# Performance work log

Measured on AMD Instinct MI355X. Metric: run time of the kernel, lower is better.

The kernel has to match this reference:

```python
import jax, jax.numpy as jnp
import numpy as np

B, N, C, O, R = 8, 1024, 768, 768, 16  # batch, tokens, in_features, out_features, rank


def setup_inputs() -> dict:
    key = jax.random.key(0)
    k1, k2, k3, k4 = jax.random.split(key, 4)
    x = jax.random.normal(k1, (B, N, C), dtype=jnp.float32)
    coef = jax.random.normal(k2, (N, R), dtype=jnp.float32)
    # params: weight (out_features, in_features, rank), bias (out_features, rank)
    weight = 0.02 * jax.random.normal(k3, (O, C, R), dtype=jnp.float32)
    bias = 0.02 * jax.random.normal(k4, (O, R), dtype=jnp.float32)
    return {"x": x, "coef": coef, "weight": weight, "bias": bias}


def reference(x, coef, weight, bias):
    # Original math: per-token weight W_n[o,c] = sum_r coef[n,r] * weight[o,c,r]
    #                out[b,n,o] = sum_c x[b,n,c] * W_n[o,c] + sum_r coef[n,r]*bias[o,r]
    # Fused form: contract in_features first, rank last; avoids the (N,O,C) tensor.
    t = jnp.einsum('bnc,ocr->bnor', x, weight)   # (B,N,O,R)
    out = jnp.einsum('bnor,nr->bno', t, coef)    # (B,N,O)
    out = out + coef @ bias.T                    # (N,O) broadcast over batch
    return out
```

## Files before the change

kernel.cpp:

```cpp
#include <hip/hip_runtime.h>

#define BB 8
#define NN 1024
#define CC 768
#define OO 768
#define RR 16
#define MM (BB*NN)
#define KK (CC*RR)
#define BM 128
#define BO 128
#define BK 64
#define KTILES (KK/BK)

typedef __bf16 bf16x8 __attribute__((ext_vector_type(8)));
typedef float  f32x4  __attribute__((ext_vector_type(4)));

__device__ static __forceinline__ void gl_lds16(const void* g, void* l) {
    __builtin_amdgcn_global_load_lds(
        (const __attribute__((address_space(1))) void*)g,
        (__attribute__((address_space(3))) void*)l,
        16, 0, 0);
}

__global__ __launch_bounds__(256) void k_prep(const float* __restrict__ w,
                                              const float* __restrict__ coef,
                                              const float* __restrict__ bias,
                                              __bf16* __restrict__ wbf,
                                              float* __restrict__ bterm) {
    long id = blockIdx.x;
    if (id < 4608) {
        long u = (id * 256 + threadIdx.x) * 8;
        float4 a = *(const float4*)(w + u);
        float4 b = *(const float4*)(w + u + 4);
        bf16x8 v = {(__bf16)a.x, (__bf16)a.y, (__bf16)a.z, (__bf16)a.w,
                    (__bf16)b.x, (__bf16)b.y, (__bf16)b.z, (__bf16)b.w};
        *(bf16x8*)(wbf + u) = v;
    } else {
        int i = (int)(id - 4608) * 256 + threadIdx.x;
        int n = i / OO, o = i - n * OO;
        float s = 0.f;
#pragma unroll
        for (int r = 0; r < RR; ++r) s += coef[n * RR + r] * bias[o * RR + r];
        bterm[i] = s;
    }
}

__global__ __launch_bounds__(256, 2) void k_gemm(const float* __restrict__ x,
                                                 const float* __restrict__ coef,
                                                 const __bf16* __restrict__ wbf,
                                                 const float* __restrict__ bterm,
                                                 float* __restrict__ out) {
    __shared__ __bf16 lA[BM * BK];
    __shared__ __bf16 lB[BO * BK];

    const int tid = threadIdx.x;

    int id    = blockIdx.x;
    int xcd   = id & 7;
    int slot  = id >> 3;
    int otile = slot >> 3;
    int mtile = xcd * 8 + (slot & 7);
    const int m0 = mtile * BM, o0 = otile * BO;

    const int am     = tid & 127;
    const int ahalf  = tid >> 7;
    const int m_glob = m0 + am;
    const int n_idx  = m_glob & (NN - 1);
    const float* xrow = x + (long)m_glob * CC;

    float cf[16];
#pragma unroll
    for (int r = 0; r < 16; r += 4) {
        float4 t4 = *(const float4*)(coef + n_idx * RR + r);
        cf[r] = t4.x; cf[r + 1] = t4.y; cf[r + 2] = t4.z; cf[r + 3] = t4.w;
    }

    const int lane = tid & 63, wave = tid >> 6;
    const int wm = (wave & 1) * 64, wo = (wave >> 1) * 64;
    const int lrow = lane & 15, quad = lane >> 4;

    f32x4 acc[4][4] = {};

    float2 x2 = *(const float2*)(xrow + 2 * ahalf);

#pragma unroll 1
    for (int kt = 0; kt < KTILES; ++kt) {
#pragma unroll
        for (int s = 0; s < 4; ++s) {
            int u = s * 256 + tid;
            int row = u >> 3, cl = u & 7;
            int g = cl ^ (row & 7);
            const __bf16* gp = wbf + (long)(o0 + row) * KK + kt * BK + g * 8;
            gl_lds16(gp, ((char*)lB) + u * 16);
        }
        float2 x2n = x2;
        if (kt + 1 < KTILES) x2n = *(const float2*)(xrow + (kt + 1) * 4 + 2 * ahalf);
#pragma unroll
        for (int ci = 0; ci < 2; ++ci) {
            float xv = (ci == 0) ? x2.x : x2.y;
            int c_local = 2 * ahalf + ci;
#pragma unroll
            for (int rh = 0; rh < 2; ++rh) {
                bf16x8 v;
#pragma unroll
                for (int j = 0; j < 8; ++j) v[j] = (__bf16)(xv * cf[rh * 8 + j]);
                int kb  = c_local * 2 + rh;
                int kbs = kb ^ (am & 7);
                *(bf16x8*)(&lA[am * BK + kbs * 8]) = v;
            }
        }
        x2 = x2n;
        __syncthreads();

#pragma unroll
        for (int ks = 0; ks < 2; ++ks) {
            bf16x8 af[4], bfr[4];
            int kb = ks * 4 + quad;
#pragma unroll
            for (int im = 0; im < 4; ++im) {
                int row = wm + im * 16 + lrow;
                af[im] = *(const bf16x8*)(&lA[row * BK + (kb ^ (row & 7)) * 8]);
            }
#pragma unroll
            for (int io = 0; io < 4; ++io) {
                int row = wo + io * 16 + lrow;
                bfr[io] = *(const bf16x8*)(&lB[row * BK + (kb ^ (row & 7)) * 8]);
            }
#pragma unroll
            for (int im = 0; im < 4; ++im)
#pragma unroll
                for (int io = 0; io < 4; ++io)
                    acc[im][io] = __builtin_amdgcn_mfma_f32_16x16x32_bf16(
                        af[im], bfr[io], acc[im][io], 0, 0, 0);
        }
        __syncthreads();
    }

    const int nbase = m0 & (NN - 1);
#pragma unroll
    for (int im = 0; im < 4; ++im) {
#pragma unroll
        for (int io = 0; io < 4; ++io) {
            int o = o0 + wo + io * 16 + lrow;
#pragma unroll
            for (int r = 0; r < 4; ++r) {
                int moff = wm + im * 16 + quad * 4 + r;
                long m = m0 + moff;
                out[m * OO + o] = acc[im][io][r] + bterm[(nbase + moff) * OO + o];
            }
        }
    }
}

__global__ void k_naive(const float* __restrict__ x, const float* __restrict__ coef,
                        const float* __restrict__ w, const float* __restrict__ bias,
                        float* __restrict__ out) {
    long i = (long)blockIdx.x * 256 + threadIdx.x;
    if (i >= (long)MM * OO) return;
    int o = (int)(i % OO);
    long m = i / OO;
    int n = (int)(m & (NN - 1));
    float cf[16];
#pragma unroll
    for (int r = 0; r < 16; ++r) cf[r] = coef[n * RR + r];
    const float* xr = x + m * CC;
    const float* wr = w + (long)o * CC * RR;
    float s = 0.f;
    for (int c = 0; c < CC; ++c) {
        float t = 0.f;
#pragma unroll
        for (int r = 0; r < 16; ++r) t += cf[r] * wr[c * RR + r];
        s += xr[c] * t;
    }
    float bs = 0.f;
#pragma unroll
    for (int r = 0; r < 16; ++r) bs += cf[r] * bias[o * RR + r];
    out[i] = s + bs;
}

extern "C" void kernel_launch(void* const* d_in, const int* in_sizes, int n_in,
                              void* d_out, int out_size, void* d_ws, size_t ws_size,
                              hipStream_t stream) {
    const float* x    = (const float*)d_in[0];
    const float* coef = (const float*)d_in[1];
    const float* w    = (const float*)d_in[2];
    const float* bias = (const float*)d_in[3];
    float* out = (float*)d_out;

    const size_t wbf_bytes = (size_t)OO * KK * sizeof(__bf16);
    const size_t bt_bytes  = (size_t)NN * OO * sizeof(float);

    if (ws_size >= wbf_bytes + bt_bytes) {
        __bf16* wbf  = (__bf16*)d_ws;
        float*  btrm = (float*)((char*)d_ws + wbf_bytes);
        k_prep<<<7680, 256, 0, stream>>>(w, coef, bias, wbf, btrm);
        k_gemm<<<384, 256, 0, stream>>>(x, coef, wbf, btrm, out);
    } else {
        k_naive<<<(int)(((long)MM * OO + 255) / 256), 256, 0, stream>>>(x, coef, w, bias, out);
    }
}
```

Measured before the change: 284.9 us.

## Build A fragments in registers, double-buffer B tile, halve output tile width

The x⊗coef A operand is no longer staged through LDS. Each lane now forms its bf16 MFMA A fragment directly in registers from a preloaded x float4 and its own coef slice, and only the weight tile goes through LDS, now double-buffered so the next tile's global-to-LDS load overlaps compute. The output tile shrinks to 64 columns, doubling the grid to 768 blocks and raising the occupancy hint to 3. The goal is to remove the A-tile LDS writes and reads and one barrier per k-step. The costs are redundant A-fragment conversion across waves, less B reuse per block and more global weight traffic.

```diff
diff --git a/kernel.cpp b/kernel.cpp
--- a/kernel.cpp
+++ b/kernel.cpp
@@ -1,14 +1,13 @@
 #include <hip/hip_runtime.h>
 
-#define BB 8
 #define NN 1024
 #define CC 768
 #define OO 768
 #define RR 16
-#define MM (BB*NN)
+#define MM 8192
 #define KK (CC*RR)
 #define BM 128
-#define BO 128
+#define BO 64
 #define BK 64
 #define KTILES (KK/BK)
 
@@ -38,20 +37,24 @@
     } else {
         int i = (int)(id - 4608) * 256 + threadIdx.x;
         int n = i / OO, o = i - n * OO;
+        const float4* cp = (const float4*)(coef + n * RR);
+        const float4* bp = (const float4*)(bias + o * RR);
         float s = 0.f;
 #pragma unroll
-        for (int r = 0; r < RR; ++r) s += coef[n * RR + r] * bias[o * RR + r];
+        for (int q = 0; q < 4; ++q) {
+            float4 c4 = cp[q], b4 = bp[q];
+            s += c4.x * b4.x + c4.y * b4.y + c4.z * b4.z + c4.w * b4.w;
+        }
         bterm[i] = s;
     }
 }
 
-__global__ __launch_bounds__(256, 2) void k_gemm(const float* __restrict__ x,
+__global__ __launch_bounds__(256, 3) void k_gemm(const float* __restrict__ x,
                                                  const float* __restrict__ coef,
                                                  const __bf16* __restrict__ wbf,
                                                  const float* __restrict__ bterm,
                                                  float* __restrict__ out) {
-    __shared__ __bf16 lA[BM * BK];
-    __shared__ __bf16 lB[BO * BK];
+    __shared__ __bf16 lB[2][BO * BK];
 
     const int tid = threadIdx.x;
 
@@ -62,91 +65,91 @@
     int mtile = xcd * 8 + (slot & 7);
     const int m0 = mtile * BM, o0 = otile * BO;
 
-    const int am     = tid & 127;
-    const int ahalf  = tid >> 7;
-    const int m_glob = m0 + am;
-    const int n_idx  = m_glob & (NN - 1);
-    const float* xrow = x + (long)m_glob * CC;
-
-    float cf[16];
-#pragma unroll
-    for (int r = 0; r < 16; r += 4) {
-        float4 t4 = *(const float4*)(coef + n_idx * RR + r);
-        cf[r] = t4.x; cf[r + 1] = t4.y; cf[r + 2] = t4.z; cf[r + 3] = t4.w;
-    }
-
     const int lane = tid & 63, wave = tid >> 6;
-    const int wm = (wave & 1) * 64, wo = (wave >> 1) * 64;
+    const int wm = (wave & 1) * 64, wo = (wave >> 1) * 32;
     const int lrow = lane & 15, quad = lane >> 4;
-
-    f32x4 acc[4][4] = {};
-
-    float2 x2 = *(const float2*)(xrow + 2 * ahalf);
-
-#pragma unroll 1
-    for (int kt = 0; kt < KTILES; ++kt) {
-#pragma unroll
-        for (int s = 0; s < 4; ++s) {
+    const int qh = quad >> 1, ql = quad & 1;
+
+    float cf8[4][8];
+    const float* xrow[4];
+#pragma unroll
+    for (int f = 0; f < 4; ++f) {
+        int m = m0 + wm + f * 16 + lrow;
+        int n = m & (NN - 1);
+#pragma unroll
+        for (int j = 0; j < 8; j += 4) {
+            float4 t = *(const float4*)(coef + n * RR + ql * 8 + j);
+            cf8[f][j] = t.x; cf8[f][j + 1] = t.y; cf8[f][j + 2] = t.z; cf8[f][j + 3] = t.w;
+        }
+        xrow[f] = x + (long)m * CC;
+    }
+
+    auto stage = [&](int kt, int buf) {
+#pragma unroll
+        for (int s = 0; s < 2; ++s) {
             int u = s * 256 + tid;
             int row = u >> 3, cl = u & 7;
             int g = cl ^ (row & 7);
             const __bf16* gp = wbf + (long)(o0 + row) * KK + kt * BK + g * 8;
-            gl_lds16(gp, ((char*)lB) + u * 16);
-        }
-        float2 x2n = x2;
-        if (kt + 1 < KTILES) x2n = *(const float2*)(xrow + (kt + 1) * 4 + 2 * ahalf);
-#pragma unroll
-        for (int ci = 0; ci < 2; ++ci) {
-            float xv = (ci == 0) ? x2.x : x2.y;
-            int c_local = 2 * ahalf + ci;
-#pragma unroll
-            for (int rh = 0; rh < 2; ++rh) {
-                bf16x8 v;
-#pragma unroll
-                for (int j = 0; j < 8; ++j) v[j] = (__bf16)(xv * cf[rh * 8 + j]);
-                int kb  = c_local * 2 + rh;
-                int kbs = kb ^ (am & 7);
-                *(bf16x8*)(&lA[am * BK + kbs * 8]) = v;
+            gl_lds16(gp, ((char*)&lB[buf][0]) + u * 16);
+        }
+    };
+
+    f32x4 acc[4][2] = {};
+
+    stage(0, 0);
+    float4 x4[4];
+#pragma unroll
+    for (int f = 0; f < 4; ++f) x4[f] = *(const float4*)(xrow[f]);
+    __syncthreads();
+
+#pragma unroll 1
+    for (int kt = 0; kt < KTILES; ++kt) {
+        const int cur = kt & 1;
+        if (kt + 1 < KTILES) stage(kt + 1, cur ^ 1);
+        float4 x4n[4];
+        const int ktn = (kt + 1 < KTILES) ? kt + 1 : kt;
+#pragma unroll
+        for (int f = 0; f < 4; ++f) x4n[f] = *(const float4*)(xrow[f] + ktn * 4);
+
+#pragma unroll
+        for (int ks = 0; ks < 2; ++ks) {
+            bf16x8 bfr[2];
+            const int kb = ks * 4 + quad;
+#pragma unroll
+            for (int io = 0; io < 2; ++io) {
+                int row = wo + io * 16 + lrow;
+                bfr[io] = *(const bf16x8*)(&lB[cur][row * BK + ((kb ^ (row & 7)) * 8)]);
             }
-        }
-        x2 = x2n;
+#pragma unroll
+            for (int f = 0; f < 4; ++f) {
+                float xs = ks ? (qh ? x4[f].w : x4[f].z)
+                              : (qh ? x4[f].y : x4[f].x);
+                bf16x8 af;
+#pragma unroll
+                for (int j = 0; j < 8; ++j) af[j] = (__bf16)(xs * cf8[f][j]);
+#pragma unroll
+                for (int io = 0; io < 2; ++io)
+                    acc[f][io] = __builtin_amdgcn_mfma_f32_16x16x32_bf16(
+                        af, bfr[io], acc[f][io], 0, 0, 0);
+            }
+        }
+#pragma unroll
+        for (int f = 0; f < 4; ++f) x4[f] = x4n[f];
         __syncthreads();
-
-#pragma unroll
-        for (int ks = 0; ks < 2; ++ks) {
-            bf16x8 af[4], bfr[4];
-            int kb = ks * 4 + quad;
-#pragma unroll
-            for (int im = 0; im < 4; ++im) {
-                int row = wm + im * 16 + lrow;
-                af[im] = *(const bf16x8*)(&lA[row * BK + (kb ^ (row & 7)) * 8]);
-            }
-#pragma unroll
-            for (int io = 0; io < 4; ++io) {
-                int row = wo + io * 16 + lrow;
-                bfr[io] = *(const bf16x8*)(&lB[row * BK + (kb ^ (row & 7)) * 8]);
-            }
-#pragma unroll
-            for (int im = 0; im < 4; ++im)
-#pragma unroll
-                for (int io = 0; io < 4; ++io)
-                    acc[im][io] = __builtin_amdgcn_mfma_f32_16x16x32_bf16(
-                        af[im], bfr[io], acc[im][io], 0, 0, 0);
-        }
-        __syncthreads();
-    }
-
-    const int nbase = m0 & (NN - 1);
-#pragma unroll
-    for (int im = 0; im < 4; ++im) {
-#pragma unroll
-        for (int io = 0; io < 4; ++io) {
+    }
+
+#pragma unroll
+    for (int f = 0; f < 4; ++f) {
+#pragma unroll
+        for (int io = 0; io < 2; ++io) {
             int o = o0 + wo + io * 16 + lrow;
 #pragma unroll
             for (int r = 0; r < 4; ++r) {
-                int moff = wm + im * 16 + quad * 4 + r;
+                int moff = wm + f * 16 + quad * 4 + r;
                 long m = m0 + moff;
-                out[m * OO + o] = acc[im][io][r] + bterm[(nbase + moff) * OO + o];
+                int n = (int)(m & (NN - 1));
+                out[m * OO + o] = acc[f][io][r] + bterm[(long)n * OO + o];
             }
         }
     }
@@ -194,7 +197,7 @@
         __bf16* wbf  = (__bf16*)d_ws;
         float*  btrm = (float*)((char*)d_ws + wbf_bytes);
         k_prep<<<7680, 256, 0, stream>>>(w, coef, bias, wbf, btrm);
-        k_gemm<<<384, 256, 0, stream>>>(x, coef, wbf, btrm, out);
+        k_gemm<<<768, 256, 0, stream>>>(x, coef, wbf, btrm, out);
     } else {
         k_naive<<<(int)(((long)MM * OO + 255) / 256), 256, 0, stream>>>(x, coef, w, bias, out);
     }
```

Result: slower. 405.5 us (+42.4%).

## Split GEMM K dimension in two with atomic accumulation into zeroed output

Applied to the files above, without the earlier changes.

Splits the long K reduction (C*R) into two halves, doubling the grid from 384 to 768 blocks so all CUs get more work and better occupancy (launch bounds raised to 3 blocks/CU). The output is zeroed in the prep kernel and each half accumulates via float atomicAdd, with only the first half adding the bias term. The bias-term computation is also vectorized with float4 loads. This trades the extra output zeroing pass and atomic write traffic for improved parallelism and load balance.

```diff
diff --git a/kernel.cpp b/kernel.cpp
--- a/kernel.cpp
+++ b/kernel.cpp
@@ -1,16 +1,17 @@
 #include <hip/hip_runtime.h>
 
-#define BB 8
 #define NN 1024
 #define CC 768
 #define OO 768
 #define RR 16
-#define MM (BB*NN)
+#define MM 8192
 #define KK (CC*RR)
 #define BM 128
 #define BO 128
 #define BK 64
 #define KTILES (KK/BK)
+#define KSPLIT 2
+#define KHALF (KTILES/KSPLIT)
 
 typedef __bf16 bf16x8 __attribute__((ext_vector_type(8)));
 typedef float  f32x4  __attribute__((ext_vector_type(4)));
@@ -26,7 +27,8 @@
                                               const float* __restrict__ coef,
                                               const float* __restrict__ bias,
                                               __bf16* __restrict__ wbf,
-                                              float* __restrict__ bterm) {
+                                              float* __restrict__ bterm,
+                                              float* __restrict__ outz) {
     long id = blockIdx.x;
     if (id < 4608) {
         long u = (id * 256 + threadIdx.x) * 8;
@@ -35,17 +37,27 @@
         bf16x8 v = {(__bf16)a.x, (__bf16)a.y, (__bf16)a.z, (__bf16)a.w,
                     (__bf16)b.x, (__bf16)b.y, (__bf16)b.z, (__bf16)b.w};
         *(bf16x8*)(wbf + u) = v;
-    } else {
+    } else if (id < 7680) {
         int i = (int)(id - 4608) * 256 + threadIdx.x;
         int n = i / OO, o = i - n * OO;
+        const float4* cp = (const float4*)(coef + n * RR);
+        const float4* bp = (const float4*)(bias + o * RR);
         float s = 0.f;
 #pragma unroll
-        for (int r = 0; r < RR; ++r) s += coef[n * RR + r] * bias[o * RR + r];
+        for (int q = 0; q < 4; ++q) {
+            float4 c4 = cp[q], b4 = bp[q];
+            s += c4.x * b4.x + c4.y * b4.y + c4.z * b4.z + c4.w * b4.w;
+        }
         bterm[i] = s;
-    }
-}
-
-__global__ __launch_bounds__(256, 2) void k_gemm(const float* __restrict__ x,
+    } else {
+        long u = ((id - 7680) * 256 + threadIdx.x) * 8;
+        float4 z = {0.f, 0.f, 0.f, 0.f};
+        *(float4*)(outz + u) = z;
+        *(float4*)(outz + u + 4) = z;
+    }
+}
+
+__global__ __launch_bounds__(256, 3) void k_gemm(const float* __restrict__ x,
                                                  const float* __restrict__ coef,
                                                  const __bf16* __restrict__ wbf,
                                                  const float* __restrict__ bterm,
@@ -58,9 +70,12 @@
     int id    = blockIdx.x;
     int xcd   = id & 7;
     int slot  = id >> 3;
-    int otile = slot >> 3;
-    int mtile = xcd * 8 + (slot & 7);
+    int kh    = slot & 1;
+    int slot2 = slot >> 1;
+    int otile = slot2 >> 3;
+    int mtile = xcd * 8 + (slot2 & 7);
     const int m0 = mtile * BM, o0 = otile * BO;
+    const int kt0 = kh * KHALF, kt1 = kt0 + KHALF;
 
     const int am     = tid & 127;
     const int ahalf  = tid >> 7;
@@ -81,10 +96,10 @@
 
     f32x4 acc[4][4] = {};
 
-    float2 x2 = *(const float2*)(xrow + 2 * ahalf);
+    float2 x2 = *(const float2*)(xrow + kt0 * 4 + 2 * ahalf);
 
 #pragma unroll 1
-    for (int kt = 0; kt < KTILES; ++kt) {
+    for (int kt = kt0; kt < kt1; ++kt) {
 #pragma unroll
         for (int s = 0; s < 4; ++s) {
             int u = s * 256 + tid;
@@ -94,7 +109,7 @@
             gl_lds16(gp, ((char*)lB) + u * 16);
         }
         float2 x2n = x2;
-        if (kt + 1 < KTILES) x2n = *(const float2*)(xrow + (kt + 1) * 4 + 2 * ahalf);
+        if (kt + 1 < kt1) x2n = *(const float2*)(xrow + (kt + 1) * 4 + 2 * ahalf);
 #pragma unroll
         for (int ci = 0; ci < 2; ++ci) {
             float xv = (ci == 0) ? x2.x : x2.y;
@@ -136,7 +151,6 @@
         __syncthreads();
     }
 
-    const int nbase = m0 & (NN - 1);
 #pragma unroll
     for (int im = 0; im < 4; ++im) {
 #pragma unroll
@@ -146,7 +160,10 @@
             for (int r = 0; r < 4; ++r) {
                 int moff = wm + im * 16 + quad * 4 + r;
                 long m = m0 + moff;
-                out[m * OO + o] = acc[im][io][r] + bterm[(nbase + moff) * OO + o];
+                int n = (int)(m & (NN - 1));
+                float v = acc[im][io][r];
+                if (kh == 0) v += bterm[(long)n * OO + o];
+                atomicAdd(&out[m * OO + o], v);
             }
         }
     }
@@ -193,8 +210,8 @@
     if (ws_size >= wbf_bytes + bt_bytes) {
         __bf16* wbf  = (__bf16*)d_ws;
         float*  btrm = (float*)((char*)d_ws + wbf_bytes);
-        k_prep<<<7680, 256, 0, stream>>>(w, coef, bias, wbf, btrm);
-        k_gemm<<<384, 256, 0, stream>>>(x, coef, wbf, btrm, out);
+        k_prep<<<10752, 256, 0, stream>>>(w, coef, bias, wbf, btrm, out);
+        k_gemm<<<768, 256, 0, stream>>>(x, coef, wbf, btrm, out);
     } else {
         k_naive<<<(int)(((long)MM * OO + 255) / 256), 256, 0, stream>>>(x, coef, w, bias, out);
     }
```

Measured after the change: 285.2 us. No clear change (+0.1%).
